# Kernel optimization log

Measured on AMD Instinct MI355X. Metric: run time of the kernel, lower is better.

The kernel has to match this reference:

```python
import jax, jax.numpy as jnp
import numpy as np

N, E, D, L, G = 50000, 640000, 128, 5, 128
BN_EPS = 1e-5

def _bn(x, g, b):
    # training-mode batchnorm over axis 0, biased variance (torch semantics)
    m = x.mean(axis=0)
    v = x.var(axis=0)
    return (x - m) * jax.lax.rsqrt(v + BN_EPS) * g + b

def setup_inputs():
    key = jax.random.key(0)
    ks = iter(jax.random.split(key, 40))
    rn = lambda shape, s=0.05: jax.random.normal(next(ks), shape, jnp.float32) * s
    inp = {}
    inp['x'] = jax.random.randint(next(ks), (N, 1), 0, 300)
    inp['edge_index'] = jax.random.randint(next(ks), (2, E), 0, N)
    inp['edge_attr'] = jax.random.normal(next(ks), (E, 7), jnp.float32)
    inp['batch'] = jnp.sort(jax.random.randint(next(ks), (N,), 0, G))
    inp['node_emb'] = rn((300, D))
    inp['vn_emb'] = jnp.zeros((1, D), jnp.float32)
    inp['eps'] = jnp.zeros((L,), jnp.float32)
    inp['edge_W'] = rn((L, 7, D)); inp['edge_b'] = rn((L, D))
    inp['W1'] = rn((L, D, 2 * D)); inp['b1'] = rn((L, 2 * D))
    inp['bn1_g'] = 1.0 + rn((L, 2 * D)); inp['bn1_b'] = rn((L, 2 * D))
    inp['W2'] = rn((L, 2 * D, D)); inp['b2'] = rn((L, D))
    inp['bn_g'] = 1.0 + rn((L, D)); inp['bn_b'] = rn((L, D))
    inp['vn_W1'] = rn((L - 1, D, 2 * D)); inp['vn_b1'] = rn((L - 1, 2 * D))
    inp['vn_bn1_g'] = 1.0 + rn((L - 1, 2 * D)); inp['vn_bn1_b'] = rn((L - 1, 2 * D))
    inp['vn_W2'] = rn((L - 1, 2 * D, D)); inp['vn_b2'] = rn((L - 1, D))
    inp['vn_bn2_g'] = 1.0 + rn((L - 1, D)); inp['vn_bn2_b'] = rn((L - 1, D))
    return inp

def reference(x, edge_index, edge_attr, batch, node_emb, vn_emb, eps,
              edge_W, edge_b, W1, b1, bn1_g, bn1_b, W2, b2, bn_g, bn_b,
              vn_W1, vn_b1, vn_bn1_g, vn_bn1_b, vn_W2, vn_b2, vn_bn2_g, vn_bn2_b):
    src, dst = edge_index[0], edge_index[1]
    h = node_emb[x[:, 0]]                      # [N, D]
    vn = jnp.broadcast_to(vn_emb, (G, D))      # virtualnode state per graph
    for l in range(L):
        h_in = h + vn[batch]                   # virtualnode broadcast
        e = edge_attr @ edge_W[l] + edge_b[l]  # [E, D]
        msg = jax.nn.relu(h_in[src] + e)       # gather + fused elementwise
        agg = jax.ops.segment_sum(msg, dst, num_segments=N)
        z = (1.0 + eps[l]) * h_in + agg
        z = jax.nn.relu(_bn(z @ W1[l] + b1[l], bn1_g[l], bn1_b[l]))
        z = _bn(z @ W2[l] + b2[l], bn_g[l], bn_b[l])
        h_out = jax.nn.relu(z) if l != L - 1 else z
        if l < L - 1:
            pooled = jax.ops.segment_sum(h_in, batch, num_segments=G)
            v = vn + pooled
            v = jax.nn.relu(_bn(v @ vn_W1[l] + vn_b1[l], vn_bn1_g[l], vn_bn1_b[l]))
            vn = jax.nn.relu(_bn(v @ vn_W2[l] + vn_b2[l], vn_bn2_g[l], vn_bn2_b[l]))
        h = h_out
    return h
```

## Files before the change

kernel.cpp:

```cpp
#include <hip/hip_runtime.h>
#include <stdint.h>

#define NN 50000
#define EE 640000
#define DD 128
#define LL 5
#define GG 128
#define D2 256

using bf16x8 = __attribute__((ext_vector_type(8))) short;
using f32x4v = __attribute__((ext_vector_type(4))) float;
using u32x4v = __attribute__((ext_vector_type(4))) unsigned int;

__device__ __forceinline__ unsigned short f2bf(float f){
  union { float f; uint32_t u; } c; c.f = f;
  uint32_t u = c.u;
  uint32_t r = (u + 0x7FFFu + ((u >> 16) & 1u)) >> 16;
  return (unsigned short)r;
}
__device__ __forceinline__ float bf2f(unsigned short u){
  union { uint32_t u; float f; } c; c.u = ((uint32_t)u) << 16; return c.f;
}
__device__ __forceinline__ float bf2f_lo(uint32_t p){
  union { uint32_t u; float f; } c; c.u = p << 16; return c.f;
}
__device__ __forceinline__ float bf2f_hi(uint32_t p){
  union { uint32_t u; float f; } c; c.u = p & 0xFFFF0000u; return c.f;
}


__global__ __launch_bounds__(256) void zero_kernel(float* p, int n){
  int i = blockIdx.x*256 + threadIdx.x;
  if (i < n) p[i] = 0.f;
}

__global__ __launch_bounds__(256) void count_kernel(const int* __restrict__ ei, int* __restrict__ counts){
  int e = blockIdx.x*256 + threadIdx.x;
  if (e < EE) atomicAdd(&counts[ei[EE + e]], 1);
}

#define SCAN_B 512
__global__ __launch_bounds__(SCAN_B) void scan1_kernel(const int* __restrict__ counts, int* __restrict__ bsums, int n){
  __shared__ int sh[SCAN_B];
  int b = blockIdx.x, t = threadIdx.x;
  int i = b*SCAN_B + t;
  sh[t] = (i < n) ? counts[i] : 0;
  __syncthreads();
  for (int s = SCAN_B/2; s > 0; s >>= 1){
    if (t < s) sh[t] += sh[t+s];
    __syncthreads();
  }
  if (t == 0) bsums[b] = sh[0];
}

__global__ void scan2_kernel(int* bsums, int nb){
  if (threadIdx.x == 0){
    int run = 0;
    for (int i = 0; i < nb; ++i){ int v = bsums[i]; bsums[i] = run; run += v; }
  }
}

__global__ __launch_bounds__(SCAN_B) void scan3_kernel(const int* __restrict__ counts, const int* __restrict__ bsums,
                                                       int* __restrict__ startp, int* __restrict__ cursor, int n){
  __shared__ int sh[SCAN_B];
  int b = blockIdx.x, t = threadIdx.x;
  int i = b*SCAN_B + t;
  int v = (i < n) ? counts[i] : 0;
  sh[t] = v;
  __syncthreads();
  for (int s = 1; s < SCAN_B; s <<= 1){
    int add = (t >= s) ? sh[t-s] : 0;
    __syncthreads();
    sh[t] += add;
    __syncthreads();
  }
  int excl = sh[t] - v + bsums[b];
  if (i < n){ startp[i] = excl; cursor[i] = excl; }
  if (i == n-1) startp[n] = excl + v;
}

__global__ __launch_bounds__(256) void fill_kernel(const int* __restrict__ ei, int* __restrict__ cursor, int* __restrict__ csr){
  int e = blockIdx.x*256 + threadIdx.x;
  if (e < EE){
    int d = ei[EE + e];
    int slot = atomicAdd(&cursor[d], 1);
    csr[slot] = e;
  }
}

__global__ __launch_bounds__(256) void egather_kernel(const int* __restrict__ csr, const int* __restrict__ ei,
                                                      const float* __restrict__ ea,
                                                      int* __restrict__ csr_src, float* __restrict__ csr_ea8){
  int s = blockIdx.x*256 + threadIdx.x;
  if (s < EE){
    int e = csr[s];
    csr_src[s] = ei[e];
    float v[8];
    #pragma unroll
    for (int k = 0; k < 7; ++k) v[k] = ea[(size_t)e*7 + k];
    v[7] = 0.f;
    #pragma unroll
    for (int k = 0; k < 8; ++k) csr_ea8[(size_t)s*8 + k] = v[k];
  }
}

__global__ __launch_bounds__(256) void wtrans_kernel(const float* __restrict__ W1, const float* __restrict__ W2,
                                                     unsigned short* __restrict__ W1T, unsigned short* __restrict__ W2T){
  int idx = blockIdx.x*256 + threadIdx.x;
  const int total = LL*DD*D2;
  if (idx < total){
    int l = idx / (DD*D2);
    int rem = idx - l*(DD*D2);
    int k = rem / D2;
    int c = rem - k*D2;
    W1T[(size_t)l*32768 + (size_t)c*128 + k] = f2bf(W1[idx]);
  } else if (idx < 2*total){
    int j = idx - total;
    int l = j / (DD*D2);
    int rem = j - l*(DD*D2);
    int k = rem / DD;
    int c = rem - k*DD;
    W2T[(size_t)l*32768 + (size_t)c*256 + k] = f2bf(W2[j]);
  }
}

__global__ __launch_bounds__(128) void init_kernel(const int* __restrict__ x, const int* __restrict__ batch,
                                                   const float* __restrict__ emb, const float* __restrict__ vn_emb,
                                                   unsigned short* __restrict__ hin_bf, float* __restrict__ vbuf0,
                                                   float* __restrict__ vn){
  int r0 = blockIdx.x*128;
  int r1 = r0 + 128; if (r1 > NN) r1 = NN;
  int d = threadIdx.x;
  float ve = vn_emb[d];
  if (blockIdx.x == 0){
    for (int g = 0; g < GG; ++g) vn[(size_t)g*DD + d] = ve;
  }
  __shared__ int sb[128];
  __shared__ int sx[128];
  if (r0 + d < r1){ sb[d] = batch[r0 + d]; sx[d] = x[r0 + d]; }
  __syncthreads();
  int curg = sb[0];
  float pacc = 0.f;
  for (int r = r0; r < r1; ++r){
    int g = sb[r - r0];
    if (g != curg){
      atomicAdd(&vbuf0[(size_t)curg*DD + d], pacc);
      pacc = 0.f; curg = g;
    }
    float hv = emb[(size_t)sx[r - r0]*DD + d] + ve;
    hin_bf[(size_t)r*DD + d] = f2bf(hv);
    pacc += hv;
  }
  atomicAdd(&vbuf0[(size_t)curg*DD + d], pacc);
}


__global__ __launch_bounds__(256) void agg3_kernel(const unsigned short* __restrict__ hin_bf,
                                                   const int* __restrict__ csr_src, const float* __restrict__ csr_ea8,
                                                   const int* __restrict__ startp,
                                                   const float* __restrict__ eW, const float* __restrict__ eb,
                                                   const float* __restrict__ eps, int l,
                                                   unsigned short* __restrict__ zout){
  const int wid  = threadIdx.x >> 6;
  const int lane = threadIdx.x & 63;
  const int node = blockIdx.x*4 + wid;
  const int s0 = startp[node], s1 = startp[node+1];
  float2 w[7];
  #pragma unroll
  for (int k = 0; k < 7; ++k) w[k] = *(const float2*)(eW + k*128 + lane*2);
  const float2 bd = *(const float2*)(eb + lane*2);
  float acc0 = 0.f, acc1 = 0.f;
  #pragma unroll 2
  for (int s = s0; s < s1; ++s){
    int src = csr_src[s];
    f32x4v a0 = *(const f32x4v*)(csr_ea8 + (size_t)s*8);
    f32x4v a1 = *(const f32x4v*)(csr_ea8 + (size_t)s*8 + 4);
    uint32_t h2 = *(const uint32_t*)(hin_bf + (size_t)src*128 + lane*2);
    float h0 = bf2f_lo(h2), h1 = bf2f_hi(h2);
    float e0 = bd.x, e1 = bd.y;
    e0 += a0[0]*w[0].x; e1 += a0[0]*w[0].y;
    e0 += a0[1]*w[1].x; e1 += a0[1]*w[1].y;
    e0 += a0[2]*w[2].x; e1 += a0[2]*w[2].y;
    e0 += a0[3]*w[3].x; e1 += a0[3]*w[3].y;
    e0 += a1[0]*w[4].x; e1 += a1[0]*w[4].y;
    e0 += a1[1]*w[5].x; e1 += a1[1]*w[5].y;
    e0 += a1[2]*w[6].x; e1 += a1[2]*w[6].y;
    float m0 = h0 + e0;
    float m1 = h1 + e1;
    acc0 += (m0 > 0.f) ? m0 : 0.f;
    acc1 += (m1 > 0.f) ? m1 : 0.f;
  }
  const float one = 1.f + eps[l];
  uint32_t hs = *(const uint32_t*)(hin_bf + (size_t)node*128 + lane*2);
  float z0 = one*bf2f_lo(hs) + acc0;
  float z1 = one*bf2f_hi(hs) + acc1;
  uint32_t out = (uint32_t)f2bf(z0) | ((uint32_t)f2bf(z1) << 16);
  *(uint32_t*)(zout + (size_t)node*128 + lane*2) = out;
}

__global__ __launch_bounds__(256) void gemm1_kernel(const unsigned short* __restrict__ A,
                                                    const unsigned short* __restrict__ BT,
                                                    const float* __restrict__ bias,
                                                    unsigned short* __restrict__ Y,
                                                    float* __restrict__ sums, float* __restrict__ sqs){
  __shared__ __align__(16) unsigned short Al[128*128];
  __shared__ __align__(16) unsigned short Bl[128*128];
  const int t = threadIdx.x;
  const int rb = blockIdx.x, cb = blockIdx.y;
  for (int it = 0; it < 8; ++it){
    int idx = it*256 + t;
    int row = idx >> 4, ch = idx & 15;
    int grow = rb*128 + row;
    u32x4v v = {0,0,0,0};
    if (grow < NN) v = *(const u32x4v*)(A + (size_t)grow*128 + ch*8);
    *(u32x4v*)((char*)Al + row*256 + ((ch*16) ^ ((row&7)<<4))) = v;
  }
  for (int it = 0; it < 8; ++it){
    int idx = it*256 + t;
    int row = idx >> 4, ch = idx & 15;
    u32x4v v = *(const u32x4v*)(BT + (size_t)(cb*128 + row)*128 + ch*8);
    *(u32x4v*)((char*)Bl + row*256 + ((ch*16) ^ ((row&7)<<4))) = v;
  }
  __syncthreads();
  const int lane = t & 63, wave = t >> 6;
  const int wm = wave >> 1, wn = wave & 1;
  const int r0 = lane & 15, kg = lane >> 4;
  f32x4v acc[4][4] = {};
  #pragma unroll
  for (int kk = 0; kk < 4; ++kk){
    const int kb = kk*64 + kg*16;
    bf16x8 a[4], b[4];
    #pragma unroll
    for (int m = 0; m < 4; ++m){
      int row = wm*64 + m*16 + r0;
      a[m] = *(const bf16x8*)((const char*)Al + row*256 + (kb ^ ((r0&7)<<4)));
    }
    #pragma unroll
    for (int n = 0; n < 4; ++n){
      int col = wn*64 + n*16 + r0;
      b[n] = *(const bf16x8*)((const char*)Bl + col*256 + (kb ^ ((r0&7)<<4)));
    }
    #pragma unroll
    for (int m = 0; m < 4; ++m)
      #pragma unroll
      for (int n = 0; n < 4; ++n)
        acc[m][n] = __builtin_amdgcn_mfma_f32_16x16x32_bf16(a[m], b[n], acc[m][n], 0, 0, 0);
  }
  #pragma unroll
  for (int n = 0; n < 4; ++n){
    const int col = cb*128 + wn*64 + n*16 + r0;
    const float bv = bias[col];
    float s = 0.f, q = 0.f;
    #pragma unroll
    for (int m = 0; m < 4; ++m){
      const int rowb = rb*128 + wm*64 + m*16 + kg*4;
      #pragma unroll
      for (int j = 0; j < 4; ++j){
        int grow = rowb + j;
        if (grow < NN){
          float v = acc[m][n][j] + bv;
          Y[(size_t)grow*256 + col] = f2bf(v);
          s += v; q += v*v;
        }
      }
    }
    s += __shfl_xor(s, 16); q += __shfl_xor(q, 16);
    s += __shfl_xor(s, 32); q += __shfl_xor(q, 32);
    if (kg == 0){ atomicAdd(&sums[col], s); atomicAdd(&sqs[col], q); }
  }
}

template<int FINAL>
__global__ __launch_bounds__(256) void gemm2_kernel(const unsigned short* __restrict__ Yin,
                                                    const float* __restrict__ sum1, const float* __restrict__ sq1,
                                                    const float* __restrict__ bg, const float* __restrict__ bb,
                                                    const unsigned short* __restrict__ BT,
                                                    const float* __restrict__ bias,
                                                    unsigned short* __restrict__ Yh, float* __restrict__ Yf,
                                                    float* __restrict__ sums, float* __restrict__ sqs){
  __shared__ __align__(16) unsigned short Al[128*128];
  __shared__ __align__(16) unsigned short Bl[128*128];
  __shared__ float s_scl[256], s_shf[256];
  const int t = threadIdx.x;
  const int rb = blockIdx.x;
  {
    const float invn = 1.f/(float)NN;
    float m = sum1[t]*invn;
    float var = sq1[t]*invn - m*m;
    var = var > 0.f ? var : 0.f;
    float sc = bg[t]*rsqrtf(var + 1e-5f);
    s_scl[t] = sc;
    s_shf[t] = bb[t] - m*sc;
  }
  const int lane = t & 63, wave = t >> 6;
  const int wm = wave >> 1, wn = wave & 1;
  const int r0 = lane & 15, kg = lane >> 4;
  f32x4v acc[4][4] = {};
  for (int kt = 0; kt < 2; ++kt){
    __syncthreads();
    for (int it = 0; it < 8; ++it){
      int idx = it*256 + t;
      int row = idx >> 4, ch = idx & 15;
      int grow = rb*128 + row;
      int c0 = kt*128 + ch*8;
      u32x4v pv = {0,0,0,0};
      if (grow < NN){
        u32x4v yv = *(const u32x4v*)(Yin + (size_t)grow*256 + c0);
        unsigned short tb[8];
        #pragma unroll
        for (int jj = 0; jj < 4; ++jj){
          uint32_t pw = yv[jj];
          float a0 = bf2f((unsigned short)(pw & 0xFFFFu));
          float a1 = bf2f((unsigned short)(pw >> 16));
          float v0 = a0*s_scl[c0 + 2*jj]     + s_shf[c0 + 2*jj];
          float v1 = a1*s_scl[c0 + 2*jj + 1] + s_shf[c0 + 2*jj + 1];
          tb[2*jj]     = f2bf(v0 > 0.f ? v0 : 0.f);
          tb[2*jj + 1] = f2bf(v1 > 0.f ? v1 : 0.f);
        }
        pv[0] = (uint32_t)tb[0] | ((uint32_t)tb[1] << 16);
        pv[1] = (uint32_t)tb[2] | ((uint32_t)tb[3] << 16);
        pv[2] = (uint32_t)tb[4] | ((uint32_t)tb[5] << 16);
        pv[3] = (uint32_t)tb[6] | ((uint32_t)tb[7] << 16);
      }
      *(u32x4v*)((char*)Al + row*256 + ((ch*16) ^ ((row&7)<<4))) = pv;
    }
    for (int it = 0; it < 8; ++it){
      int idx = it*256 + t;
      int row = idx >> 4, ch = idx & 15;
      u32x4v v = *(const u32x4v*)(BT + (size_t)row*256 + kt*128 + ch*8);
      *(u32x4v*)((char*)Bl + row*256 + ((ch*16) ^ ((row&7)<<4))) = v;
    }
    __syncthreads();
    #pragma unroll
    for (int kk = 0; kk < 4; ++kk){
      const int kb = kk*64 + kg*16;
      bf16x8 a[4], b[4];
      #pragma unroll
      for (int m = 0; m < 4; ++m){
        int row = wm*64 + m*16 + r0;
        a[m] = *(const bf16x8*)((const char*)Al + row*256 + (kb ^ ((r0&7)<<4)));
      }
      #pragma unroll
      for (int n = 0; n < 4; ++n){
        int col = wn*64 + n*16 + r0;
        b[n] = *(const bf16x8*)((const char*)Bl + col*256 + (kb ^ ((r0&7)<<4)));
      }
      #pragma unroll
      for (int m = 0; m < 4; ++m)
        #pragma unroll
        for (int n = 0; n < 4; ++n)
          acc[m][n] = __builtin_amdgcn_mfma_f32_16x16x32_bf16(a[m], b[n], acc[m][n], 0, 0, 0);
    }
  }
  #pragma unroll
  for (int n = 0; n < 4; ++n){
    const int col = wn*64 + n*16 + r0;
    const float bv = bias[col];
    float s = 0.f, q = 0.f;
    #pragma unroll
    for (int m = 0; m < 4; ++m){
      const int rowb = rb*128 + wm*64 + m*16 + kg*4;
      #pragma unroll
      for (int j = 0; j < 4; ++j){
        int grow = rowb + j;
        if (grow < NN){
          float v = acc[m][n][j] + bv;
          if (FINAL) Yf[(size_t)grow*128 + col] = v;
          else       Yh[(size_t)grow*128 + col] = f2bf(v);
          s += v; q += v*v;
        }
      }
    }
    s += __shfl_xor(s, 16); q += __shfl_xor(q, 16);
    s += __shfl_xor(s, 32); q += __shfl_xor(q, 32);
    if (kg == 0){ atomicAdd(&sums[col], s); atomicAdd(&sqs[col], q); }
  }
}

__global__ __launch_bounds__(128) void happly_fused_kernel(const unsigned short* __restrict__ y2h,
                                                           const float* __restrict__ sum2, const float* __restrict__ sq2,
                                                           const float* __restrict__ bg, const float* __restrict__ bb,
                                                           const float* __restrict__ vn, const int* __restrict__ batch,
                                                           unsigned short* __restrict__ hin_bf, float* __restrict__ vbuf_next){
  int r0 = blockIdx.x*128;
  int r1 = r0 + 128; if (r1 > NN) r1 = NN;
  int d = threadIdx.x;
  const float invn = 1.f/(float)NN;
  float m = sum2[d]*invn;
  float var = sq2[d]*invn - m*m;
  var = var > 0.f ? var : 0.f;
  float sc = bg[d]*rsqrtf(var + 1e-5f);
  float sh = bb[d] - m*sc;
  __shared__ int sb[128];
  if (r0 + d < r1) sb[d] = batch[r0 + d];
  __syncthreads();
  int curg = sb[0];
  float vnv = vn[(size_t)curg*DD + d];
  float pacc = 0.f;
  for (int r = r0; r < r1; ++r){
    int g = sb[r - r0];
    if (g != curg){
      atomicAdd(&vbuf_next[(size_t)curg*DD + d], pacc);
      pacc = 0.f; curg = g;
      vnv = vn[(size_t)curg*DD + d];
    }
    float y = bf2f(y2h[(size_t)r*DD + d]);
    float v = y*sc + sh;
    v = v > 0.f ? v : 0.f;
    float hv = v + vnv;
    hin_bf[(size_t)r*DD + d] = f2bf(hv);
    pacc += hv;
  }
  atomicAdd(&vbuf_next[(size_t)curg*DD + d], pacc);
}

__global__ __launch_bounds__(256) void happly_final_kernel(float* __restrict__ y,
                                                           const float* __restrict__ sum2, const float* __restrict__ sq2,
                                                           const float* __restrict__ bg, const float* __restrict__ bb){
  int idx = blockIdx.x*256 + threadIdx.x;
  if (idx >= NN*32) return;
  int c4 = idx & 31;
  const float invn = 1.f/(float)NN;
  f32x4v yv = *(const f32x4v*)(y + (size_t)idx*4);
  f32x4v o;
  #pragma unroll
  for (int j = 0; j < 4; ++j){
    int c = c4*4 + j;
    float m = sum2[c]*invn;
    float var = sq2[c]*invn - m*m;
    var = var > 0.f ? var : 0.f;
    float sc = bg[c]*rsqrtf(var + 1e-5f);
    o[j] = (yv[j] - m)*sc + bb[c];
  }
  *(f32x4v*)(y + (size_t)idx*4) = o;
}

__global__ __launch_bounds__(256) void vmlp1_kernel(const float* __restrict__ vn, const float* __restrict__ vbufl,
                                                    const float* __restrict__ W, const float* __restrict__ bias,
                                                    float* __restrict__ Yo,
                                                    float* __restrict__ sums, float* __restrict__ sqs){
  __shared__ float vrow[128];
  int r = blockIdx.x, c = threadIdx.x;
  if (c < 128) vrow[c] = vn[r*128 + c] + vbufl[r*128 + c];
  __syncthreads();
  float acc = 0.f;
  #pragma unroll 8
  for (int k = 0; k < 128; ++k) acc += vrow[k]*W[k*256 + c];
  float y = acc + bias[c];
  Yo[r*256 + c] = y;
  atomicAdd(&sums[c], y);
  atomicAdd(&sqs[c], y*y);
}

__global__ __launch_bounds__(128) void vmlp2_kernel(const float* __restrict__ Yin,
                                                    const float* __restrict__ sumv1, const float* __restrict__ sqv1,
                                                    const float* __restrict__ vg, const float* __restrict__ vb,
                                                    const float* __restrict__ W, const float* __restrict__ bias,
                                                    float* __restrict__ Yo,
                                                    float* __restrict__ sums, float* __restrict__ sqs){
  __shared__ float arow[256];
  __shared__ float s_scl[256], s_shf[256];
  int r = blockIdx.x, c = threadIdx.x;
  const float invg = 1.f/(float)GG;
  for (int k = c; k < 256; k += 128){
    float m = sumv1[k]*invg;
    float var = sqv1[k]*invg - m*m;
    var = var > 0.f ? var : 0.f;
    float sc = vg[k]*rsqrtf(var + 1e-5f);
    s_scl[k] = sc;
    s_shf[k] = vb[k] - m*sc;
  }
  __syncthreads();
  for (int k = c; k < 256; k += 128){
    float a = Yin[r*256 + k]*s_scl[k] + s_shf[k];
    arow[k] = a > 0.f ? a : 0.f;
  }
  __syncthreads();
  float acc = 0.f;
  #pragma unroll 8
  for (int k = 0; k < 256; ++k) acc += arow[k]*W[k*128 + c];
  float y = acc + bias[c];
  Yo[r*128 + c] = y;
  atomicAdd(&sums[c], y);
  atomicAdd(&sqs[c], y*y);
}

__global__ __launch_bounds__(256) void va_kernel(const float* __restrict__ yv2,
                                                 const float* __restrict__ sumv2, const float* __restrict__ sqv2,
                                                 const float* __restrict__ vg, const float* __restrict__ vb,
                                                 float* __restrict__ vn){
  int idx = blockIdx.x*256 + threadIdx.x;
  if (idx < GG*128){
    int c = idx & 127;
    const float invg = 1.f/(float)GG;
    float m = sumv2[c]*invg;
    float var = sqv2[c]*invg - m*m;
    var = var > 0.f ? var : 0.f;
    float sc = vg[c]*rsqrtf(var + 1e-5f);
    float v = (yv2[idx] - m)*sc + vb[c];
    vn[idx] = v > 0.f ? v : 0.f;
  }
}


extern "C" void kernel_launch(void* const* d_in, const int* in_sizes, int n_in,
                              void* d_out, int out_size, void* d_ws, size_t ws_size,
                              hipStream_t stream){
  const int*   x         = (const int*)  d_in[0];
  const int*   ei        = (const int*)  d_in[1];
  const float* edge_attr = (const float*)d_in[2];
  const int*   batch     = (const int*)  d_in[3];
  const float* node_emb  = (const float*)d_in[4];
  const float* vn_emb    = (const float*)d_in[5];
  const float* eps       = (const float*)d_in[6];
  const float* edge_W    = (const float*)d_in[7];
  const float* edge_b    = (const float*)d_in[8];
  const float* W1        = (const float*)d_in[9];
  const float* b1        = (const float*)d_in[10];
  const float* bn1_g     = (const float*)d_in[11];
  const float* bn1_b     = (const float*)d_in[12];
  const float* W2        = (const float*)d_in[13];
  const float* b2        = (const float*)d_in[14];
  const float* bn_g      = (const float*)d_in[15];
  const float* bn_b      = (const float*)d_in[16];
  const float* vn_W1     = (const float*)d_in[17];
  const float* vn_b1     = (const float*)d_in[18];
  const float* vn_bn1_g  = (const float*)d_in[19];
  const float* vn_bn1_b  = (const float*)d_in[20];
  const float* vn_W2     = (const float*)d_in[21];
  const float* vn_b2     = (const float*)d_in[22];
  const float* vn_bn2_g  = (const float*)d_in[23];
  const float* vn_bn2_b  = (const float*)d_in[24];
  float* hout = (float*)d_out;

  char* ws = (char*)d_ws;
  size_t off = 0;
  auto alloc = [&](size_t bytes)->char*{
    char* p = ws + off; off += (bytes + 255) & ~(size_t)255; return p;
  };
  unsigned short* hin_bf = (unsigned short*)alloc((size_t)NN*DD*2);
  unsigned short* zy     = (unsigned short*)alloc((size_t)NN*DD*2);
  unsigned short* y1h    = (unsigned short*)alloc((size_t)NN*D2*2);
  float*          vn     = (float*)         alloc((size_t)GG*DD*4);
  float*          yv1    = (float*)         alloc((size_t)GG*D2*4);
  float*          yv2    = (float*)         alloc((size_t)GG*DD*4);
  unsigned short* W1T    = (unsigned short*)alloc((size_t)LL*D2*DD*2);
  unsigned short* W2T    = (unsigned short*)alloc((size_t)LL*D2*DD*2);
  const int STATS_F = LL*8*256;
  const int VBUF_F  = 5*GG*DD;
  const int ZTOT    = STATS_F + VBUF_F + NN;
  float* zeroreg = (float*)alloc((size_t)ZTOT*4);
  float* stats_all = zeroreg;
  float* vbuf_all  = zeroreg + STATS_F;
  int*   counts    = (int*)(zeroreg + STATS_F + VBUF_F);
  int*   startp = (int*)  alloc((size_t)(NN+1)*4);
  int*   cursor = (int*)  alloc((size_t)NN*4);
  int*   csr    = (int*)  alloc((size_t)EE*4);
  int*   bsums  = (int*)  alloc(128*4);
  int*   csr_src= (int*)  alloc((size_t)EE*4);
  float* csr_ea8= (float*)alloc((size_t)EE*8*4);

  const int nb_scan = (NN + SCAN_B - 1)/SCAN_B;
  const int row_blocks = (NN + 127)/128;
  const int ew_blocks = (NN*32 + 255)/256;

  zero_kernel<<<(ZTOT + 255)/256, 256, 0, stream>>>(zeroreg, ZTOT);
  count_kernel<<<EE/256, 256, 0, stream>>>(ei, counts);
  scan1_kernel<<<nb_scan, SCAN_B, 0, stream>>>(counts, bsums, NN);
  scan2_kernel<<<1, 64, 0, stream>>>(bsums, nb_scan);
  scan3_kernel<<<nb_scan, SCAN_B, 0, stream>>>(counts, bsums, startp, cursor, NN);
  fill_kernel<<<EE/256, 256, 0, stream>>>(ei, cursor, csr);
  egather_kernel<<<EE/256, 256, 0, stream>>>(csr, ei, edge_attr, csr_src, csr_ea8);
  wtrans_kernel<<<(2*LL*DD*D2 + 255)/256, 256, 0, stream>>>(W1, W2, W1T, W2T);
  init_kernel<<<row_blocks, 128, 0, stream>>>(x, batch, node_emb, vn_emb, hin_bf, vbuf_all, vn);

  for (int l = 0; l < LL; ++l){
    float* st    = stats_all + (size_t)l*8*256;
    float* sum1  = st + 0*256, *sq1  = st + 1*256;
    float* sum2  = st + 2*256, *sq2  = st + 3*256;
    float* sumv1 = st + 4*256, *sqv1 = st + 5*256;
    float* sumv2 = st + 6*256, *sqv2 = st + 7*256;

    agg3_kernel<<<NN/4, 256, 0, stream>>>(hin_bf, csr_src, csr_ea8, startp,
                                          edge_W + (size_t)l*7*DD, edge_b + (size_t)l*DD, eps, l, zy);
    gemm1_kernel<<<dim3(row_blocks, 2), 256, 0, stream>>>(zy, W1T + (size_t)l*32768,
                                                          b1 + (size_t)l*D2, y1h, sum1, sq1);
    if (l != LL-1){
      gemm2_kernel<0><<<row_blocks, 256, 0, stream>>>(y1h, sum1, sq1,
                                                      bn1_g + (size_t)l*D2, bn1_b + (size_t)l*D2,
                                                      W2T + (size_t)l*32768, b2 + (size_t)l*DD,
                                                      zy, nullptr, sum2, sq2);
      float* vbufl = vbuf_all + (size_t)l*GG*DD;
      float* vbufn = vbuf_all + (size_t)(l+1)*GG*DD;
      vmlp1_kernel<<<GG, 256, 0, stream>>>(vn, vbufl, vn_W1 + (size_t)l*DD*D2, vn_b1 + (size_t)l*D2,
                                           yv1, sumv1, sqv1);
      vmlp2_kernel<<<GG, 128, 0, stream>>>(yv1, sumv1, sqv1,
                                           vn_bn1_g + (size_t)l*D2, vn_bn1_b + (size_t)l*D2,
                                           vn_W2 + (size_t)l*D2*DD, vn_b2 + (size_t)l*DD,
                                           yv2, sumv2, sqv2);
      va_kernel<<<(GG*DD + 255)/256, 256, 0, stream>>>(yv2, sumv2, sqv2,
                                                       vn_bn2_g + (size_t)l*DD, vn_bn2_b + (size_t)l*DD, vn);
      happly_fused_kernel<<<row_blocks, 128, 0, stream>>>(zy, sum2, sq2,
                                                          bn_g + (size_t)l*DD, bn_b + (size_t)l*DD,
                                                          vn, batch, hin_bf, vbufn);
    } else {
      gemm2_kernel<1><<<row_blocks, 256, 0, stream>>>(y1h, sum1, sq1,
                                                      bn1_g + (size_t)l*D2, bn1_b + (size_t)l*D2,
                                                      W2T + (size_t)l*32768, b2 + (size_t)l*DD,
                                                      nullptr, hout, sum2, sq2);
      happly_final_kernel<<<ew_blocks, 256, 0, stream>>>(hout, sum2, sq2,
                                                         bn_g + (size_t)l*DD, bn_b + (size_t)l*DD);
    }
  }
  (void)in_sizes; (void)n_in; (void)out_size; (void)ws_size;
}
```

Measured before the change: 1.295 ms.

## Pad CSR segments to multiples of four and store edge attributes in bf16

Per-node CSR segments are padded to multiples of 4 edges. Pad slots point to a sentinel row of hin_bf filled with bf16 -inf, so their ReLU messages are zero. This lets the aggregation kernel load four source indices and four packed bf16 edge-attribute vectors per iteration, keeping four gathers in flight. Edge attributes are stored as bf16 (half the bytes), and the fill and gather passes merge into one kernel that writes in CSR order, which drops the intermediate csr array. The costs are reduced edge-attribute precision, an extra init kernel over the padded buffer, and a hard-coded maximum padded size.

Measured after the change: 1.263 ms. 1.03x faster.

```diff
diff --git a/kernel.cpp b/kernel.cpp
--- a/kernel.cpp
+++ b/kernel.cpp
@@ -7,6 +7,7 @@
 #define LL 5
 #define GG 128
 #define D2 256
+#define CSRP_MAX 790016
 
 using bf16x8 = __attribute__((ext_vector_type(8))) short;
 using f32x4v = __attribute__((ext_vector_type(4))) float;
@@ -44,7 +45,7 @@
   __shared__ int sh[SCAN_B];
   int b = blockIdx.x, t = threadIdx.x;
   int i = b*SCAN_B + t;
-  sh[t] = (i < n) ? counts[i] : 0;
+  sh[t] = (i < n) ? ((counts[i] + 3) & ~3) : 0;
   __syncthreads();
   for (int s = SCAN_B/2; s > 0; s >>= 1){
     if (t < s) sh[t] += sh[t+s];
@@ -65,7 +66,7 @@
   __shared__ int sh[SCAN_B];
   int b = blockIdx.x, t = threadIdx.x;
   int i = b*SCAN_B + t;
-  int v = (i < n) ? counts[i] : 0;
+  int v = (i < n) ? ((counts[i] + 3) & ~3) : 0;
   sh[t] = v;
   __syncthreads();
   for (int s = 1; s < SCAN_B; s <<= 1){
@@ -79,28 +80,33 @@
   if (i == n-1) startp[n] = excl + v;
 }
 
-__global__ __launch_bounds__(256) void fill_kernel(const int* __restrict__ ei, int* __restrict__ cursor, int* __restrict__ csr){
+__global__ __launch_bounds__(256) void csrinit_kernel(int* __restrict__ csr_src, unsigned short* __restrict__ csr_eah){
+  int i = blockIdx.x*256 + threadIdx.x;
+  if (i < CSRP_MAX){
+    csr_src[i] = NN;
+    u32x4v z = {0,0,0,0};
+    *(u32x4v*)(csr_eah + (size_t)i*8) = z;
+  }
+}
+
+__global__ __launch_bounds__(256) void fillcvt_kernel(const int* __restrict__ ei, const float* __restrict__ ea,
+                                                      int* __restrict__ cursor,
+                                                      int* __restrict__ csr_src, unsigned short* __restrict__ csr_eah){
   int e = blockIdx.x*256 + threadIdx.x;
   if (e < EE){
     int d = ei[EE + e];
     int slot = atomicAdd(&cursor[d], 1);
-    csr[slot] = e;
-  }
-}
-
-__global__ __launch_bounds__(256) void egather_kernel(const int* __restrict__ csr, const int* __restrict__ ei,
-                                                      const float* __restrict__ ea,
-                                                      int* __restrict__ csr_src, float* __restrict__ csr_ea8){
-  int s = blockIdx.x*256 + threadIdx.x;
-  if (s < EE){
-    int e = csr[s];
-    csr_src[s] = ei[e];
-    float v[8];
+    csr_src[slot] = ei[e];
+    unsigned short t[8];
     #pragma unroll
-    for (int k = 0; k < 7; ++k) v[k] = ea[(size_t)e*7 + k];
-    v[7] = 0.f;
-    #pragma unroll
-    for (int k = 0; k < 8; ++k) csr_ea8[(size_t)s*8 + k] = v[k];
+    for (int k = 0; k < 7; ++k) t[k] = f2bf(ea[(size_t)e*7 + k]);
+    t[7] = 0;
+    u32x4v pv;
+    pv[0] = (uint32_t)t[0] | ((uint32_t)t[1] << 16);
+    pv[1] = (uint32_t)t[2] | ((uint32_t)t[3] << 16);
+    pv[2] = (uint32_t)t[4] | ((uint32_t)t[5] << 16);
+    pv[3] = (uint32_t)t[6] | ((uint32_t)t[7] << 16);
+    *(u32x4v*)(csr_eah + (size_t)slot*8) = pv;
   }
 }
 
@@ -134,6 +140,7 @@
   float ve = vn_emb[d];
   if (blockIdx.x == 0){
     for (int g = 0; g < GG; ++g) vn[(size_t)g*DD + d] = ve;
+    hin_bf[(size_t)NN*DD + d] = 0xFF80u;
   }
   __shared__ int sb[128];
   __shared__ int sx[128];
@@ -155,8 +162,9 @@
 }
 
 
-__global__ __launch_bounds__(256) void agg3_kernel(const unsigned short* __restrict__ hin_bf,
-                                                   const int* __restrict__ csr_src, const float* __restrict__ csr_ea8,
+__global__ __launch_bounds__(256) void agg4_kernel(const unsigned short* __restrict__ hin_bf,
+                                                   const int* __restrict__ csr_src,
+                                                   const unsigned short* __restrict__ csr_eah,
                                                    const int* __restrict__ startp,
                                                    const float* __restrict__ eW, const float* __restrict__ eb,
                                                    const float* __restrict__ eps, int l,
@@ -170,25 +178,31 @@
   for (int k = 0; k < 7; ++k) w[k] = *(const float2*)(eW + k*128 + lane*2);
   const float2 bd = *(const float2*)(eb + lane*2);
   float acc0 = 0.f, acc1 = 0.f;
-  #pragma unroll 2
-  for (int s = s0; s < s1; ++s){
-    int src = csr_src[s];
-    f32x4v a0 = *(const f32x4v*)(csr_ea8 + (size_t)s*8);
-    f32x4v a1 = *(const f32x4v*)(csr_ea8 + (size_t)s*8 + 4);
-    uint32_t h2 = *(const uint32_t*)(hin_bf + (size_t)src*128 + lane*2);
-    float h0 = bf2f_lo(h2), h1 = bf2f_hi(h2);
-    float e0 = bd.x, e1 = bd.y;
-    e0 += a0[0]*w[0].x; e1 += a0[0]*w[0].y;
-    e0 += a0[1]*w[1].x; e1 += a0[1]*w[1].y;
-    e0 += a0[2]*w[2].x; e1 += a0[2]*w[2].y;
-    e0 += a0[3]*w[3].x; e1 += a0[3]*w[3].y;
-    e0 += a1[0]*w[4].x; e1 += a1[0]*w[4].y;
-    e0 += a1[1]*w[5].x; e1 += a1[1]*w[5].y;
-    e0 += a1[2]*w[6].x; e1 += a1[2]*w[6].y;
-    float m0 = h0 + e0;
-    float m1 = h1 + e1;
-    acc0 += (m0 > 0.f) ? m0 : 0.f;
-    acc1 += (m1 > 0.f) ? m1 : 0.f;
+  for (int s = s0; s < s1; s += 4){
+    const int4 sv = *(const int4*)(csr_src + s);
+    u32x4v p0 = *(const u32x4v*)(csr_eah + (size_t)s*8);
+    u32x4v p1 = *(const u32x4v*)(csr_eah + (size_t)s*8 + 8);
+    u32x4v p2 = *(const u32x4v*)(csr_eah + (size_t)s*8 + 16);
+    u32x4v p3 = *(const u32x4v*)(csr_eah + (size_t)s*8 + 24);
+    uint32_t h0 = *(const uint32_t*)(hin_bf + (size_t)sv.x*128 + lane*2);
+    uint32_t h1 = *(const uint32_t*)(hin_bf + (size_t)sv.y*128 + lane*2);
+    uint32_t h2 = *(const uint32_t*)(hin_bf + (size_t)sv.z*128 + lane*2);
+    uint32_t h3 = *(const uint32_t*)(hin_bf + (size_t)sv.w*128 + lane*2);
+#define EDGE(P, H) { \
+    float a0v = bf2f_lo(P[0]), a1v = bf2f_hi(P[0]); \
+    float a2v = bf2f_lo(P[1]), a3v = bf2f_hi(P[1]); \
+    float a4v = bf2f_lo(P[2]), a5v = bf2f_hi(P[2]); \
+    float a6v = bf2f_lo(P[3]); \
+    float e0 = bd.x + a0v*w[0].x + a1v*w[1].x + a2v*w[2].x + a3v*w[3].x + a4v*w[4].x + a5v*w[5].x + a6v*w[6].x; \
+    float e1 = bd.y + a0v*w[0].y + a1v*w[1].y + a2v*w[2].y + a3v*w[3].y + a4v*w[4].y + a5v*w[5].y + a6v*w[6].y; \
+    float m0 = bf2f_lo(H) + e0, m1 = bf2f_hi(H) + e1; \
+    acc0 += (m0 > 0.f) ? m0 : 0.f; \
+    acc1 += (m1 > 0.f) ? m1 : 0.f; }
+    EDGE(p0, h0)
+    EDGE(p1, h1)
+    EDGE(p2, h2)
+    EDGE(p3, h3)
+#undef EDGE
   }
   const float one = 1.f + eps[l];
   uint32_t hs = *(const uint32_t*)(hin_bf + (size_t)node*128 + lane*2);
@@ -538,7 +552,7 @@
   auto alloc = [&](size_t bytes)->char*{
     char* p = ws + off; off += (bytes + 255) & ~(size_t)255; return p;
   };
-  unsigned short* hin_bf = (unsigned short*)alloc((size_t)NN*DD*2);
+  unsigned short* hin_bf = (unsigned short*)alloc((size_t)(NN+1)*DD*2);
   unsigned short* zy     = (unsigned short*)alloc((size_t)NN*DD*2);
   unsigned short* y1h    = (unsigned short*)alloc((size_t)NN*D2*2);
   float*          vn     = (float*)         alloc((size_t)GG*DD*4);
@@ -555,22 +569,21 @@
   int*   counts    = (int*)(zeroreg + STATS_F + VBUF_F);
   int*   startp = (int*)  alloc((size_t)(NN+1)*4);
   int*   cursor = (int*)  alloc((size_t)NN*4);
-  int*   csr    = (int*)  alloc((size_t)EE*4);
   int*   bsums  = (int*)  alloc(128*4);
-  int*   csr_src= (int*)  alloc((size_t)EE*4);
-  float* csr_ea8= (float*)alloc((size_t)EE*8*4);
+  int*   csr_src= (int*)  alloc((size_t)CSRP_MAX*4);
+  unsigned short* csr_eah = (unsigned short*)alloc((size_t)CSRP_MAX*8*2);
 
   const int nb_scan = (NN + SCAN_B - 1)/SCAN_B;
   const int row_blocks = (NN + 127)/128;
   const int ew_blocks = (NN*32 + 255)/256;
 
   zero_kernel<<<(ZTOT + 255)/256, 256, 0, stream>>>(zeroreg, ZTOT);
+  csrinit_kernel<<<(CSRP_MAX + 255)/256, 256, 0, stream>>>(csr_src, csr_eah);
   count_kernel<<<EE/256, 256, 0, stream>>>(ei, counts);
   scan1_kernel<<<nb_scan, SCAN_B, 0, stream>>>(counts, bsums, NN);
   scan2_kernel<<<1, 64, 0, stream>>>(bsums, nb_scan);
   scan3_kernel<<<nb_scan, SCAN_B, 0, stream>>>(counts, bsums, startp, cursor, NN);
-  fill_kernel<<<EE/256, 256, 0, stream>>>(ei, cursor, csr);
-  egather_kernel<<<EE/256, 256, 0, stream>>>(csr, ei, edge_attr, csr_src, csr_ea8);
+  fillcvt_kernel<<<EE/256, 256, 0, stream>>>(ei, edge_attr, cursor, csr_src, csr_eah);
   wtrans_kernel<<<(2*LL*DD*D2 + 255)/256, 256, 0, stream>>>(W1, W2, W1T, W2T);
   init_kernel<<<row_blocks, 128, 0, stream>>>(x, batch, node_emb, vn_emb, hin_bf, vbuf_all, vn);
 
@@ -581,7 +594,7 @@
     float* sumv1 = st + 4*256, *sqv1 = st + 5*256;
     float* sumv2 = st + 6*256, *sqv2 = st + 7*256;
 
-    agg3_kernel<<<NN/4, 256, 0, stream>>>(hin_bf, csr_src, csr_ea8, startp,
+    agg4_kernel<<<NN/4, 256, 0, stream>>>(hin_bf, csr_src, csr_eah, startp,
                                           edge_W + (size_t)l*7*DD, edge_b + (size_t)l*DD, eps, l, zy);
     gemm1_kernel<<<dim3(row_blocks, 2), 256, 0, stream>>>(zy, W1T + (size_t)l*32768,
                                                           b1 + (size_t)l*D2, y1h, sum1, sq1);
```
